# Performance work log

Hardware: AMD Instinct MI355X
Metric: run time of the kernel (lower is better)

The kernel has to match this reference:

```python
import jax, jax.numpy as jnp
import numpy as np

EPS = 1e-12
CLAMP = 1.0 - 1e-6


def _hamilton(a, b):
    r1, i1, j1, k1 = a
    r2, i2, j2, k2 = b
    return (r1 * r2 - i1 * i2 - j1 * j2 - k1 * k2,
            r1 * i2 + i1 * r2 + j1 * k2 - k1 * j2,
            r1 * j2 - i1 * k2 + j1 * r2 + k1 * i2,
            r1 * k2 + i1 * j2 - j1 * i2 + k1 * r2)


def _chained_prod(r, i, j, k):
    """Left-to-right Hamilton product along the last axis via tree reduction."""
    n = r.shape[-1]
    m = 1 << (n - 1).bit_length()  # next power of two
    if m != n:
        pad = [(0, 0)] * (r.ndim - 1) + [(0, m - n)]
        # pad with identity quaternion (1,0,0,0)
        r = jnp.pad(r, pad, constant_values=1.0)
        i = jnp.pad(i, pad)
        j = jnp.pad(j, pad)
        k = jnp.pad(k, pad)
    q = (r, i, j, k)
    while q[0].shape[-1] > 1:
        a = tuple(t[..., 0::2] for t in q)
        b = tuple(t[..., 1::2] for t in q)
        q = _hamilton(a, b)
    return tuple(t[..., 0] for t in q)


def reference(x, weight, bias):
    # x: (B, T, 4*C_in) laid out as [r | i | j | k]; weight: (C_out, C_in); bias: (C_out,)
    r, i, j, k = jnp.split(x, 4, axis=-1)  # each (B, T, C_in)
    norm_v = jnp.sqrt(i * i + j * j + k * k + EPS)
    theta = jnp.arccos(jnp.clip(r, -CLAMP, CLAMP))  # (B, T, C_in)
    # quaternion power: angle scaled by weight, shifted by bias -> (B, T, C_out, C_in)
    theta = weight * theta[..., None, :] + bias[:, None]
    mul = jnp.sin(theta) / norm_v[..., None, :]
    qr = jnp.cos(theta)
    qi = i[..., None, :] * mul
    qj = j[..., None, :] * mul
    qk = k[..., None, :] * mul
    # chained Hamilton product over C_in -> (B, T, C_out)
    pr, pi, pj, pk = _chained_prod(qr, qi, qj, qk)
    # quaternion normalize
    n = jnp.sqrt(pr * pr + pi * pi + pj * pj + pk * pk + EPS)
    return jnp.concatenate([pr / n, pi / n, pj / n, pk / n], axis=-1)  # (B, T, 4*C_out)


def setup_inputs() -> dict:
    key = jax.random.key(0)
    k1, k2, k3 = jax.random.split(key, 3)
    C_in, C_out = 64, 128
    x = jax.random.normal(k1, (16, 128, 4 * C_in), dtype=jnp.float32)
    a = float(np.sqrt(6.0 / (C_in + C_out)))  # xavier bound
    weight = jax.random.uniform(k2, (C_out, C_in), minval=-a, maxval=a, dtype=jnp.float32)
    bias = jax.random.uniform(k3, (C_out,), minval=-a, maxval=a, dtype=jnp.float32)
    return {"x": x, "weight": weight, "bias": bias}
```

## Files before the change

kernel.cpp:

```cpp
#include <hip/hip_runtime.h>
#include <math.h>


#define C_IN   64
#define C_OUT  128
#define POS_PER_BLOCK 4
#define BLOCK  (POS_PER_BLOCK * C_OUT)
#define WT_STRIDE (C_OUT + 1)

#define INV_2PI 0.15915494309189535f

__global__ __launch_bounds__(BLOCK, 4) void qpu_kernel(
    const float* __restrict__ x,
    const float* __restrict__ weight,
    const float* __restrict__ bias,
    float* __restrict__ out,
    int P)
{
    __shared__ float  w_t[C_IN * WT_STRIDE];
    __shared__ float4 pre[POS_PER_BLOCK][C_IN];

    const int tid = threadIdx.x;

    {
        const float4* w4 = (const float4*)weight;
        #pragma unroll
        for (int idx = tid; idx < (C_OUT * C_IN) / 4; idx += BLOCK) {
            const float4 v = w4[idx];
            const int o  = idx >> 4;
            const int c0 = (idx & 15) * 4;
            w_t[(c0 + 0) * WT_STRIDE + o] = v.x;
            w_t[(c0 + 1) * WT_STRIDE + o] = v.y;
            w_t[(c0 + 2) * WT_STRIDE + o] = v.z;
            w_t[(c0 + 3) * WT_STRIDE + o] = v.w;
        }
    }

    const int sub = tid >> 7;
    const int o   = tid & 127;
    const int pos = blockIdx.x * POS_PER_BLOCK + sub;
    const bool valid = (pos < P);

    if (valid && o < C_IN) {
        const int c = o;
        const float* xb = x + (size_t)pos * (4 * C_IN);
        const float r = xb[c];
        const float i = xb[C_IN + c];
        const float j = xb[2 * C_IN + c];
        const float k = xb[3 * C_IN + c];
        const float rc = fminf(fmaxf(r, -0.999999f), 0.999999f);
        const float th0 = acosf(rc);
        const float inv = rsqrtf(fmaf(i, i, fmaf(j, j, fmaf(k, k, 1e-12f))));
        pre[sub][c] = make_float4(th0, i * inv, j * inv, k * inv);
    }
    __syncthreads();

    if (!valid) return;

    const float b_o = bias[o] * INV_2PI;

    float pr = 1.0f, pi = 0.0f, pj = 0.0f, pk = 0.0f;

    #pragma unroll 8
    for (int c = 0; c < C_IN; ++c) {
        const float4 p4 = pre[sub][c];
        const float  w  = w_t[c * WT_STRIDE + o];
        const float rev = fmaf(w * INV_2PI, p4.x, b_o);
        const float s  = __builtin_amdgcn_sinf(rev);
        const float ct = __builtin_amdgcn_cosf(rev);
        const float qr = ct;
        const float qi = p4.y * s;
        const float qj = p4.z * s;
        const float qk = p4.w * s;
        const float nr = pr * qr - pi * qi - pj * qj - pk * qk;
        const float ni = pr * qi + pi * qr + pj * qk - pk * qj;
        const float nj = pr * qj - pi * qk + pj * qr + pk * qi;
        const float nk = pr * qk + pi * qj - pj * qi + pk * qr;
        pr = nr; pi = ni; pj = nj; pk = nk;
    }

    const float invn = rsqrtf(fmaf(pr, pr, fmaf(pi, pi, fmaf(pj, pj, fmaf(pk, pk, 1e-12f)))));
    float* ob = out + (size_t)pos * (4 * C_OUT);
    ob[o]             = pr * invn;
    ob[C_OUT + o]     = pi * invn;
    ob[2 * C_OUT + o] = pj * invn;
    ob[3 * C_OUT + o] = pk * invn;
}

extern "C" void kernel_launch(void* const* d_in, const int* in_sizes, int n_in,
                              void* d_out, int out_size, void* d_ws, size_t ws_size,
                              hipStream_t stream) {
    const float* x      = (const float*)d_in[0];
    const float* weight = (const float*)d_in[1];
    const float* bias   = (const float*)d_in[2];
    float* out          = (float*)d_out;

    const int P = in_sizes[0] / (4 * C_IN);
    const int grid = (P + POS_PER_BLOCK - 1) / POS_PER_BLOCK;

    qpu_kernel<<<grid, BLOCK, 0, stream>>>(x, weight, bias, out, P);
}
```

Measured before the change: 72.28 us.

## Process two output channels per thread with packed float2 math

Each thread now computes two adjacent output channels using float2 vector types, halving the block to 256 threads. The goal is to let the compiler emit packed FP32 instructions (v_pk_fma/v_pk_mul) for the Hamilton product and to amortize the per-channel shared loads of the precomputed input quaternion across two outputs. Weight storage in shared memory is re-padded for 8-byte reads, and output stores become 8-byte vector writes. The cost is more registers per thread and fewer threads in flight, and the sin/cos transcendental calls stay scalar.

```diff
diff --git a/kernel.cpp b/kernel.cpp
--- a/kernel.cpp
+++ b/kernel.cpp
@@ -2,25 +2,29 @@
 #include <math.h>
 
 
+typedef float v2f __attribute__((ext_vector_type(2)));
+
 #define C_IN   64
 #define C_OUT  128
 #define POS_PER_BLOCK 4
-#define BLOCK  (POS_PER_BLOCK * C_OUT)
-#define WT_STRIDE (C_OUT + 1)
+#define BLOCK  (POS_PER_BLOCK * 64)
+#define WSTR2  (C_OUT / 2 + 1)
 
 #define INV_2PI 0.15915494309189535f
 
-__global__ __launch_bounds__(BLOCK, 4) void qpu_kernel(
+__global__ __launch_bounds__(BLOCK, 2) void qpu_kernel(
     const float* __restrict__ x,
     const float* __restrict__ weight,
     const float* __restrict__ bias,
     float* __restrict__ out,
     int P)
 {
-    __shared__ float  w_t[C_IN * WT_STRIDE];
+    __shared__ float  w_s[C_IN * WSTR2 * 2];
     __shared__ float4 pre[POS_PER_BLOCK][C_IN];
 
-    const int tid = threadIdx.x;
+    const int tid  = threadIdx.x;
+    const int lane = tid & 63;
+    const int sub  = tid >> 6;
 
     {
         const float4* w4 = (const float4*)weight;
@@ -29,20 +33,18 @@
             const float4 v = w4[idx];
             const int o  = idx >> 4;
             const int c0 = (idx & 15) * 4;
-            w_t[(c0 + 0) * WT_STRIDE + o] = v.x;
-            w_t[(c0 + 1) * WT_STRIDE + o] = v.y;
-            w_t[(c0 + 2) * WT_STRIDE + o] = v.z;
-            w_t[(c0 + 3) * WT_STRIDE + o] = v.w;
+            w_s[(c0 + 0) * (2 * WSTR2) + o] = v.x;
+            w_s[(c0 + 1) * (2 * WSTR2) + o] = v.y;
+            w_s[(c0 + 2) * (2 * WSTR2) + o] = v.z;
+            w_s[(c0 + 3) * (2 * WSTR2) + o] = v.w;
         }
     }
 
-    const int sub = tid >> 7;
-    const int o   = tid & 127;
     const int pos = blockIdx.x * POS_PER_BLOCK + sub;
     const bool valid = (pos < P);
 
-    if (valid && o < C_IN) {
-        const int c = o;
+    if (valid) {
+        const int c = lane;
         const float* xb = x + (size_t)pos * (4 * C_IN);
         const float r = xb[c];
         const float i = xb[C_IN + c];
@@ -57,34 +59,43 @@
 
     if (!valid) return;
 
-    const float b_o = bias[o] * INV_2PI;
+    const v2f b2 = ((const v2f*)bias)[lane] * INV_2PI;
+    const v2f* __restrict__ w2 = (const v2f*)w_s;
 
-    float pr = 1.0f, pi = 0.0f, pj = 0.0f, pk = 0.0f;
+    v2f pr = 1.0f, pi = 0.0f, pj = 0.0f, pk = 0.0f;
 
     #pragma unroll 8
     for (int c = 0; c < C_IN; ++c) {
         const float4 p4 = pre[sub][c];
-        const float  w  = w_t[c * WT_STRIDE + o];
-        const float rev = fmaf(w * INV_2PI, p4.x, b_o);
-        const float s  = __builtin_amdgcn_sinf(rev);
-        const float ct = __builtin_amdgcn_cosf(rev);
-        const float qr = ct;
-        const float qi = p4.y * s;
-        const float qj = p4.z * s;
-        const float qk = p4.w * s;
-        const float nr = pr * qr - pi * qi - pj * qj - pk * qk;
-        const float ni = pr * qi + pi * qr + pj * qk - pk * qj;
-        const float nj = pr * qj - pi * qk + pj * qr + pk * qi;
-        const float nk = pr * qk + pi * qj - pj * qi + pk * qr;
+        const v2f    w  = w2[c * WSTR2 + lane];
+        const float  thr = p4.x * INV_2PI;
+        const v2f    rev = w * thr + b2;
+        v2f s, ct;
+        s.x  = __builtin_amdgcn_sinf(rev.x);
+        s.y  = __builtin_amdgcn_sinf(rev.y);
+        ct.x = __builtin_amdgcn_cosf(rev.x);
+        ct.y = __builtin_amdgcn_cosf(rev.y);
+        const v2f qi = p4.y * s;
+        const v2f qj = p4.z * s;
+        const v2f qk = p4.w * s;
+        const v2f nr = pr * ct - pi * qi - pj * qj - pk * qk;
+        const v2f ni = pr * qi + pi * ct + pj * qk - pk * qj;
+        const v2f nj = pr * qj - pi * qk + pj * ct + pk * qi;
+        const v2f nk = pr * qk + pi * qj - pj * qi + pk * ct;
         pr = nr; pi = ni; pj = nj; pk = nk;
     }
 
-    const float invn = rsqrtf(fmaf(pr, pr, fmaf(pi, pi, fmaf(pj, pj, fmaf(pk, pk, 1e-12f)))));
+    const v2f n2 = pr * pr + pi * pi + pj * pj + pk * pk + 1e-12f;
+    v2f invn;
+    invn.x = rsqrtf(n2.x);
+    invn.y = rsqrtf(n2.y);
+    pr *= invn; pi *= invn; pj *= invn; pk *= invn;
+
     float* ob = out + (size_t)pos * (4 * C_OUT);
-    ob[o]             = pr * invn;
-    ob[C_OUT + o]     = pi * invn;
-    ob[2 * C_OUT + o] = pj * invn;
-    ob[3 * C_OUT + o] = pk * invn;
+    ((v2f*)(ob              ))[lane] = pr;
+    ((v2f*)(ob +     C_OUT  ))[lane] = pi;
+    ((v2f*)(ob + 2 * C_OUT  ))[lane] = pj;
+    ((v2f*)(ob + 3 * C_OUT  ))[lane] = pk;
 }
 
 extern "C" void kernel_launch(void* const* d_in, const int* in_sizes, int n_in,
```

Result: faster. 67.40 us (-6.8%).
